# Kernel tuning notes

Hardware: AMD Instinct MI355X
Metric: run time of the kernel (lower is better)

The kernel has to match this reference:

```python
import jax, jax.numpy as jnp
import numpy as np

WH, WW = 14, 14
NUM_HEADS = 12
HEAD_DIM = 64
HIDDEN = NUM_HEADS * HEAD_DIM
SEQ = WH * WW + 1  # 197, includes cls token
NUM_REL = (2 * WH - 1) * (2 * WW - 1) + 3  # 732


def _relative_position_index(wh, ww):
    # Static numpy computation, identical to BeitRelativePositionBias buffer
    coords = np.stack(np.meshgrid(np.arange(wh), np.arange(ww), indexing='ij'))  # [2, wh, ww]
    flat = coords.reshape(2, -1)  # [2, wh*ww]
    rel = flat[:, :, None] - flat[:, None, :]  # [2, N, N]
    rel = rel.transpose(1, 2, 0).astype(np.int64)  # [N, N, 2]
    rel[..., 0] += wh - 1
    rel[..., 1] += ww - 1
    rel[..., 0] *= 2 * ww - 1
    nrd = (2 * wh - 1) * (2 * ww - 1) + 3
    idx = np.zeros((wh * ww + 1, wh * ww + 1), dtype=np.int64)
    idx[1:, 1:] = rel.sum(-1)
    idx[0, :] = nrd - 3
    idx[:, 0] = nrd - 2
    idx[0, 0] = nrd - 1
    return idx

_REL_IDX = jnp.asarray(_relative_position_index(WH, WW))  # [SEQ, SEQ]


def setup_inputs() -> dict:
    key = jax.random.key(0)
    ks = jax.random.split(key, 7)
    B = 64
    s = 1.0 / np.sqrt(HIDDEN)
    return {
        'hidden_states': jax.random.normal(ks[0], (B, SEQ, HIDDEN), jnp.float32),
        'Wq': jax.random.normal(ks[1], (HIDDEN, HIDDEN), jnp.float32) * s,
        'bq': jax.random.normal(ks[2], (HIDDEN,), jnp.float32) * 0.02,
        'Wk': jax.random.normal(ks[3], (HIDDEN, HIDDEN), jnp.float32) * s,
        'Wv': jax.random.normal(ks[4], (HIDDEN, HIDDEN), jnp.float32) * s,
        'bv': jax.random.normal(ks[5], (HIDDEN,), jnp.float32) * 0.02,
        'bias_table': jax.random.normal(ks[6], (NUM_REL, NUM_HEADS), jnp.float32) * 0.02,
    }


def reference(hidden_states, Wq, bq, Wk, Wv, bv, bias_table):
    B, S, D = hidden_states.shape
    H, Dh = NUM_HEADS, HEAD_DIM

    def heads(x):  # [B,S,D] -> [B,H,S,Dh]
        return x.reshape(B, S, H, Dh).transpose(0, 2, 1, 3)

    q = heads(hidden_states @ Wq + bq)
    k = heads(hidden_states @ Wk)           # key projection has no bias
    v = heads(hidden_states @ Wv + bv)

    scores = jnp.einsum('bhqd,bhkd->bhqk', q, k) / jnp.sqrt(jnp.float32(Dh))
    # relative position bias: gather [SEQ,SEQ,H] -> [H,SEQ,SEQ]
    rel_bias = bias_table[_REL_IDX].transpose(2, 0, 1)
    scores = scores + rel_bias[None]

    probs = jax.nn.softmax(scores, axis=-1)  # dropout prob = 0 (eval)
    ctx = jnp.einsum('bhqk,bhkd->bhqd', probs, v)
    ctx = ctx.transpose(0, 2, 1, 3).reshape(B, S, D)
    return ctx
```

## Files before the change

### kernel.cpp

```cpp
#include <hip/hip_runtime.h>
#include <hip/hip_bf16.h>
#include <stdint.h>

typedef unsigned short u16;
typedef __attribute__((ext_vector_type(4))) float f32x4;
typedef __attribute__((ext_vector_type(8))) short s16x8;
typedef __attribute__((ext_vector_type(4))) unsigned short u16x4;
typedef __attribute__((ext_vector_type(4))) float fvec4;

#define NH 12
#define DH 64
#define HID 768
#define SEQ 197
#define VP 224
#define NREL 732
#define BATCH 64
#define MROWS (BATCH*SEQ)
#define NCAT (3*HID)
#define BK 64
#define MT 99
#define NT 18
#define NWG (MT*NT)
#define AWG (768*13)
#define QKSTRIDE (SEQ*DH)

#define PB_X 4728
#define PB_W (PB_X + 432)
#define PB_B (PB_W + 9)
#define PB_E (PB_B + 2028)

static __device__ __forceinline__ u16 f2bf(float f) {
  union { float f; uint32_t u; } v; v.f = f;
  uint32_t u = v.u;
  return (u16)((u + 0x7FFFu + ((u >> 16) & 1u)) >> 16);
}
static __device__ __forceinline__ float bf2f(u16 v) {
  union { uint32_t u; float f; } x; x.u = ((uint32_t)v) << 16; return x.f;
}

__global__ __launch_bounds__(256) void prep_all(const float* __restrict__ x,
                                                const float* __restrict__ Wq, const float* __restrict__ Wk,
                                                const float* __restrict__ Wv, const float* __restrict__ bq,
                                                const float* __restrict__ bv, const float* __restrict__ btab,
                                                u16* __restrict__ xb, u16* __restrict__ Wt,
                                                float* __restrict__ bc, u16* __restrict__ Bxt) {
  __shared__ float t[64][65];
  const int bi = blockIdx.x;
  const int tid = threadIdx.x;
  if (bi < PB_X) {
    int i = bi * 256 + tid;
    fvec4 a = ((const fvec4*)x)[2 * i];
    fvec4 b = ((const fvec4*)x)[2 * i + 1];
    s16x8 r;
    r[0] = (short)f2bf(a[0]); r[1] = (short)f2bf(a[1]); r[2] = (short)f2bf(a[2]); r[3] = (short)f2bf(a[3]);
    r[4] = (short)f2bf(b[0]); r[5] = (short)f2bf(b[1]); r[6] = (short)f2bf(b[2]); r[7] = (short)f2bf(b[3]);
    ((s16x8*)xb)[i] = r;
  } else if (bi < PB_W) {
    int f = bi - PB_X;
    int n0 = (f % 36) * 64, k0 = (f / 36) * 64;
    int m = n0 / HID;
    const float* W = (m == 0) ? Wq : ((m == 1) ? Wk : Wv);
    int nn0 = n0 - m * HID;
    for (int i = tid; i < 64 * 64; i += 256) {
      int r = i >> 6, c = i & 63;
      t[r][c] = W[(size_t)(k0 + r) * HID + nn0 + c];
    }
    __syncthreads();
    for (int i = tid; i < 64 * 64; i += 256) {
      int r = i >> 6, c = i & 63;
      Wt[(size_t)(n0 + r) * HID + k0 + c] = f2bf(t[c][r]);
    }
  } else if (bi < PB_B) {
    int i = (bi - PB_W) * 256 + tid;
    if (i < NCAT) {
      int m = i / HID, r = i - m * HID;
      bc[i] = (m == 0) ? bq[r] : ((m == 2) ? bv[r] : 0.f);
    }
  } else {
    int i = (bi - PB_B) * 256 + tid;
    int h = i / (208 * 208);
    int r = i - h * 208 * 208;
    int k = r / 208, q = r - k * 208;
    float v;
    if (k >= SEQ) v = -1e30f;
    else if (q >= SEQ) v = 0.f;
    else {
      int idx;
      if (q == 0) idx = (k == 0) ? 731 : 729;
      else if (k == 0) idx = 730;
      else {
        int iq = (q - 1) / 14, jq = (q - 1) % 14;
        int ik = (k - 1) / 14, jk = (k - 1) % 14;
        idx = (iq - ik + 13) * 27 + (jq - jk + 13);
      }
      v = btab[(size_t)idx * NH + h];
    }
    Bxt[i] = f2bf(v);
  }
}

static __device__ __forceinline__ void stage128(const u16* __restrict__ gbase, int grow0, int growmax,
                                                u16* lds, int w, int l) {
#pragma unroll
  for (int i = 0; i < 4; ++i) {
    int ch = w * 4 + i;
    int r = ch * 8 + (l >> 3);
    int grow = grow0 + r; if (grow > growmax) grow = growmax;
    int c = (l & 7) ^ (l >> 3);
    const u16* g = gbase + (size_t)grow * HID + c * 8;
    __builtin_amdgcn_global_load_lds((const __attribute__((address_space(1))) void*)g,
                                     (__attribute__((address_space(3))) void*)(lds + ch * 512),
                                     16, 0, 0);
  }
}

static __device__ __forceinline__ void compute128(const u16* As, const u16* Bs, int wr, int wc,
                                                  int li, int lg, f32x4 acc[4][4]) {
#pragma unroll
  for (int kk = 0; kk < 2; ++kk) {
    s16x8 af[4], bf[4];
#pragma unroll
    for (int mi = 0; mi < 4; ++mi) {
      int r = wr * 64 + mi * 16 + li;
      int c = (kk * 4 + lg) ^ (r & 7);
      af[mi] = *(const s16x8*)((const char*)As + r * 128 + c * 16);
    }
#pragma unroll
    for (int ni = 0; ni < 4; ++ni) {
      int r = wc * 64 + ni * 16 + li;
      int c = (kk * 4 + lg) ^ (r & 7);
      bf[ni] = *(const s16x8*)((const char*)Bs + r * 128 + c * 16);
    }
#pragma unroll
    for (int mi = 0; mi < 4; ++mi)
#pragma unroll
      for (int ni = 0; ni < 4; ++ni)
        acc[mi][ni] = __builtin_amdgcn_mfma_f32_16x16x32_bf16(af[mi], bf[ni], acc[mi][ni], 0, 0, 0);
  }
}

__global__ __launch_bounds__(256, 2) void qkv_gemm(const u16* __restrict__ Xb, const u16* __restrict__ Wt,
                                                   const float* __restrict__ bc, u16* __restrict__ Qw,
                                                   u16* __restrict__ Kw, u16* __restrict__ Vt) {
  __shared__ u16 LDSU[32768];
  u16* As0 = LDSU;
  u16* Bs0 = LDSU + 8192;
  u16* As1 = LDSU + 16384;
  u16* Bs1 = LDSU + 24576;
  const int tid = threadIdx.x;
  const int w = tid >> 6, l = tid & 63;
  const int wr = w >> 1, wc = w & 1;
  const int lg = l >> 4, li = l & 15;

  const int lin = blockIdx.x;
  const int xcd = lin & 7;
  const int pos = lin >> 3;
  const int work = (xcd < 6 ? xcd * 223 : 6 * 223 + (xcd - 6) * 222) + pos;
  const int mt = work / NT, nt = work - mt * NT;
  const int arow0 = mt * 128, brow0 = nt * 128;

  f32x4 acc[4][4] = {};

  stage128(Xb, arow0, MROWS - 1, As0, w, l);
  stage128(Wt, brow0, NCAT - 1, Bs0, w, l);
  __syncthreads();

  for (int kt2 = 0; kt2 < 6; ++kt2) {
    const int kt = kt2 * 2;
    stage128(Xb + (kt + 1) * BK, arow0, MROWS - 1, As1, w, l);
    stage128(Wt + (kt + 1) * BK, brow0, NCAT - 1, Bs1, w, l);
    compute128(As0, Bs0, wr, wc, li, lg, acc);
    __syncthreads();
    if (kt2 < 5) {
      stage128(Xb + (kt + 2) * BK, arow0, MROWS - 1, As0, w, l);
      stage128(Wt + (kt + 2) * BK, brow0, NCAT - 1, Bs0, w, l);
    }
    compute128(As1, Bs1, wr, wc, li, lg, acc);
    __syncthreads();
  }

  const int mblk = nt / 6;
  float bcv[4];
#pragma unroll
  for (int ni = 0; ni < 4; ++ni) bcv[ni] = bc[brow0 + wc * 64 + ni * 16 + li];

  if (mblk < 2) {
    u16* __restrict__ dst = (mblk == 0) ? Qw : Kw;
    const float scale = (mblk == 0) ? 0.125f : 1.0f;
    int hv[4], dv[4];
#pragma unroll
    for (int ni = 0; ni < 4; ++ni) {
      int cloc = brow0 - mblk * HID + wc * 64 + ni * 16 + li;
      hv[ni] = cloc >> 6; dv[ni] = cloc & 63;
    }
#pragma unroll
    for (int mi = 0; mi < 4; ++mi) {
#pragma unroll
      for (int j = 0; j < 4; ++j) {
        int row = arow0 + wr * 64 + mi * 16 + lg * 4 + j;
        if (row < MROWS) {
          int b = row / SEQ, s = row - b * SEQ;
#pragma unroll
          for (int ni = 0; ni < 4; ++ni)
            dst[((size_t)(b * NH + hv[ni]) * SEQ + s) * DH + dv[ni]] = f2bf((acc[mi][ni][j] + bcv[ni]) * scale);
        }
      }
    }
  } else {
#pragma unroll
    for (int mi = 0; mi < 4; ++mi) {
#pragma unroll
      for (int ni = 0; ni < 4; ++ni) {
        u16x4 pk;
#pragma unroll
        for (int j = 0; j < 4; ++j) pk[j] = f2bf(acc[mi][ni][j] + bcv[ni]);
        *(u16x4*)&LDSU[w * 4352 + (ni * 16 + li) * 68 + mi * 16 + lg * 4] = pk;
      }
    }
    __syncthreads();
    const int cw0 = brow0 - 2 * HID;
#pragma unroll 4
    for (int p = 0; p < 64; ++p) {
      int i = p * 256 + tid;
      int r = i & 127, c = i >> 7;
      int wq = ((r >> 6) << 1) | (c >> 6);
      u16 v = LDSU[wq * 4352 + (c & 63) * 68 + (r & 63)];
      int row = arow0 + r;
      if (row < MROWS) {
        int b = row / SEQ, s = row - b * SEQ;
        int cl = cw0 + c;
        int h = cl >> 6, d = cl & 63;
        Vt[((size_t)(b * NH + h) * DH + d) * VP + s] = v;
      }
    }
  }
}

__global__ __launch_bounds__(64, 3) void attn(const u16* __restrict__ Qw, const u16* __restrict__ Kw,
                                              const u16* __restrict__ Vt, const u16* __restrict__ Bxt,
                                              float* __restrict__ out) {
  __shared__ u16 P[16 * 232];
  const int l = threadIdx.x;
  const int lg = l >> 4, li = l & 15;
  const int lin = blockIdx.x;
  const int work = (lin & 7) * (AWG / 8) + (lin >> 3);
  const int bh = work / 13, qf = work - bh * 13;
  const int b = bh / NH, h = bh - b * NH;

  for (int t = l; t < 16 * 24; t += 64) {
    int rr = t / 24, cc = t - rr * 24;
    P[rr * 232 + 208 + cc] = 0;
  }

  const u16* Qb = Qw + (size_t)bh * QKSTRIDE;
  const u16* Kb = Kw + (size_t)bh * QKSTRIDE;
  const u16* Vb = Vt + (size_t)bh * DH * VP;
  const u16* Bhp = Bxt + (size_t)h * 208 * 208 + qf * 16 + lg * 4;

  s16x8 a0 = *(const s16x8*)(Qb + (size_t)(qf * 16 + li) * DH + lg * 8);
  s16x8 a1 = *(const s16x8*)(Qb + (size_t)(qf * 16 + li) * DH + 32 + lg * 8);

  u16x4 bb[13];
#pragma unroll
  for (int kf = 0; kf < 13; ++kf)
    bb[kf] = *(const u16x4*)(Bhp + (size_t)(kf * 16 + li) * 208);

  s16x8 kb0[3], kb1[3];
#pragma unroll
  for (int p = 0; p < 3; ++p) {
    kb0[p] = *(const s16x8*)(Kb + (size_t)(p * 16 + li) * DH + lg * 8);
    kb1[p] = *(const s16x8*)(Kb + (size_t)(p * 16 + li) * DH + 32 + lg * 8);
  }
  f32x4 S[13];
#pragma unroll
  for (int kf = 0; kf < 13; ++kf) {
    const int slot = kf % 3;
    f32x4 c = {};
    c = __builtin_amdgcn_mfma_f32_16x16x32_bf16(a0, kb0[slot], c, 0, 0, 0);
    c = __builtin_amdgcn_mfma_f32_16x16x32_bf16(a1, kb1[slot], c, 0, 0, 0);
    if (kf + 3 < 13) {
      kb0[slot] = *(const s16x8*)(Kb + (size_t)((kf + 3) * 16 + li) * DH + lg * 8);
      kb1[slot] = *(const s16x8*)(Kb + (size_t)((kf + 3) * 16 + li) * DH + 32 + lg * 8);
    }
#pragma unroll
    for (int j = 0; j < 4; ++j)
      S[kf][j] = c[j] + bf2f(bb[kf][j]);
  }

  float rinv[4];
#pragma unroll
  for (int j = 0; j < 4; ++j) {
    float m = S[0][j];
#pragma unroll
    for (int kf = 1; kf < 13; ++kf) m = fmaxf(m, S[kf][j]);
    m = fmaxf(m, __shfl_xor(m, 1));
    m = fmaxf(m, __shfl_xor(m, 2));
    m = fmaxf(m, __shfl_xor(m, 4));
    m = fmaxf(m, __shfl_xor(m, 8));
    float sum = 0.f;
#pragma unroll
    for (int kf = 0; kf < 13; ++kf) {
      float p = __expf(S[kf][j] - m);
      S[kf][j] = p;
      sum += p;
    }
    sum += __shfl_xor(sum, 1);
    sum += __shfl_xor(sum, 2);
    sum += __shfl_xor(sum, 4);
    sum += __shfl_xor(sum, 8);
    rinv[j] = 1.0f / sum;
  }

#pragma unroll
  for (int kf = 0; kf < 13; ++kf)
#pragma unroll
    for (int j = 0; j < 4; ++j)
      P[(lg * 4 + j) * 232 + kf * 16 + li] = f2bf(S[kf][j]);

  s16x8 vb[4];
#pragma unroll
  for (int p = 0; p < 4; ++p)
    vb[p] = *(const s16x8*)(Vb + (size_t)((p / 7) * 16 + li) * VP + (p % 7) * 32 + lg * 8);
  f32x4 o[4];
#pragma unroll
  for (int nf = 0; nf < 4; ++nf) {
    f32x4 c = {};
#pragma unroll
    for (int t = 0; t < 7; ++t) {
      const int u = nf * 7 + t, slot = u & 3;
      s16x8 pa = *(const s16x8*)(&P[li * 232 + t * 32 + lg * 8]);
      c = __builtin_amdgcn_mfma_f32_16x16x32_bf16(pa, vb[slot], c, 0, 0, 0);
      if (u + 4 < 28) {
        const int u2 = u + 4;
        vb[slot] = *(const s16x8*)(Vb + (size_t)((u2 / 7) * 16 + li) * VP + (u2 % 7) * 32 + lg * 8);
      }
    }
    o[nf] = c;
  }
#pragma unroll
  for (int nf = 0; nf < 4; ++nf) {
#pragma unroll
    for (int j = 0; j < 4; ++j) {
      int q = qf * 16 + lg * 4 + j;
      if (q < SEQ)
        out[((size_t)(b * SEQ + q)) * HID + h * DH + nf * 16 + li] = o[nf][j] * rinv[j];
    }
  }
}

extern "C" void kernel_launch(void* const* d_in, const int* in_sizes, int n_in,
                              void* d_out, int out_size, void* d_ws, size_t ws_size,
                              hipStream_t stream) {
  const float* hidden = (const float*)d_in[0];
  const float* Wq = (const float*)d_in[1];
  const float* bq = (const float*)d_in[2];
  const float* Wk = (const float*)d_in[3];
  const float* Wv = (const float*)d_in[4];
  const float* bv = (const float*)d_in[5];
  const float* btab = (const float*)d_in[6];
  float* out = (float*)d_out;

  char* ws = (char*)d_ws;
  u16* Xb  = (u16*)(ws);
  u16* Wt  = (u16*)(ws + 19365888);
  float* bc = (float*)(ws + 22904832);
  u16* Bxt = (u16*)(ws + 22914048);
  u16* Qw  = (u16*)(ws + 23952512);
  u16* Kw  = (u16*)(ws + 43322496);
  u16* Vt  = (u16*)(ws + 62692480);

  prep_all<<<dim3(PB_E), dim3(256), 0, stream>>>(hidden, Wq, Wk, Wv, bq, bv, btab, Xb, Wt, bc, Bxt);
  qkv_gemm<<<dim3(NWG), dim3(256), 0, stream>>>(Xb, Wt, bc, Qw, Kw, Vt);
  attn<<<dim3(AWG), dim3(64), 0, stream>>>(Qw, Kw, Vt, Bxt, out);
}
```

Measured before the change: 135.7 us.

## Share K across query tiles via swizzled LDS in per-head attention blocks

The attention kernel now launches one 2-wave block per (batch, head) instead of one single-wave block per (batch, head, query tile). The whole K matrix for the head is staged once into LDS with direct global-to-LDS loads and an XOR swizzle. Each wave then loops over its query tiles, reading K from LDS rather than re-fetching it from global memory for every tile. This removes redundant K traffic, but it cuts the grid to 768 small blocks and serialises query tiles within each wave, which lowers occupancy and latency hiding.

```diff
diff --git a/kernel.cpp b/kernel.cpp
--- a/kernel.cpp
+++ b/kernel.cpp
@@ -21,7 +21,6 @@
 #define MT 99
 #define NT 18
 #define NWG (MT*NT)
-#define AWG (768*13)
 #define QKSTRIDE (SEQ*DH)
 
 #define PB_X 4728
@@ -236,114 +235,124 @@
   }
 }
 
-__global__ __launch_bounds__(64, 3) void attn(const u16* __restrict__ Qw, const u16* __restrict__ Kw,
-                                              const u16* __restrict__ Vt, const u16* __restrict__ Bxt,
-                                              float* __restrict__ out) {
-  __shared__ u16 P[16 * 232];
-  const int l = threadIdx.x;
+__global__ __launch_bounds__(128, 2) void attn(const u16* __restrict__ Qw, const u16* __restrict__ Kw,
+                                               const u16* __restrict__ Vt, const u16* __restrict__ Bxt,
+                                               float* __restrict__ out) {
+  __shared__ u16 Klds[208 * 64];
+  __shared__ u16 P[2][16 * 232];
+  const int tid = threadIdx.x;
+  const int w = tid >> 6, l = tid & 63;
   const int lg = l >> 4, li = l & 15;
   const int lin = blockIdx.x;
-  const int work = (lin & 7) * (AWG / 8) + (lin >> 3);
-  const int bh = work / 13, qf = work - bh * 13;
+  const int bh = (lin & 7) * 96 + (lin >> 3);
   const int b = bh / NH, h = bh - b * NH;
-
-  for (int t = l; t < 16 * 24; t += 64) {
-    int rr = t / 24, cc = t - rr * 24;
-    P[rr * 232 + 208 + cc] = 0;
-  }
 
   const u16* Qb = Qw + (size_t)bh * QKSTRIDE;
   const u16* Kb = Kw + (size_t)bh * QKSTRIDE;
   const u16* Vb = Vt + (size_t)bh * DH * VP;
-  const u16* Bhp = Bxt + (size_t)h * 208 * 208 + qf * 16 + lg * 4;
-
-  s16x8 a0 = *(const s16x8*)(Qb + (size_t)(qf * 16 + li) * DH + lg * 8);
-  s16x8 a1 = *(const s16x8*)(Qb + (size_t)(qf * 16 + li) * DH + 32 + lg * 8);
-
-  u16x4 bb[13];
-#pragma unroll
-  for (int kf = 0; kf < 13; ++kf)
-    bb[kf] = *(const u16x4*)(Bhp + (size_t)(kf * 16 + li) * 208);
-
-  s16x8 kb0[3], kb1[3];
-#pragma unroll
-  for (int p = 0; p < 3; ++p) {
-    kb0[p] = *(const s16x8*)(Kb + (size_t)(p * 16 + li) * DH + lg * 8);
-    kb1[p] = *(const s16x8*)(Kb + (size_t)(p * 16 + li) * DH + 32 + lg * 8);
-  }
-  f32x4 S[13];
-#pragma unroll
-  for (int kf = 0; kf < 13; ++kf) {
-    const int slot = kf % 3;
-    f32x4 c = {};
-    c = __builtin_amdgcn_mfma_f32_16x16x32_bf16(a0, kb0[slot], c, 0, 0, 0);
-    c = __builtin_amdgcn_mfma_f32_16x16x32_bf16(a1, kb1[slot], c, 0, 0, 0);
-    if (kf + 3 < 13) {
-      kb0[slot] = *(const s16x8*)(Kb + (size_t)((kf + 3) * 16 + li) * DH + lg * 8);
-      kb1[slot] = *(const s16x8*)(Kb + (size_t)((kf + 3) * 16 + li) * DH + 32 + lg * 8);
-    }
-#pragma unroll
-    for (int j = 0; j < 4; ++j)
-      S[kf][j] = c[j] + bf2f(bb[kf][j]);
-  }
-
-  float rinv[4];
-#pragma unroll
-  for (int j = 0; j < 4; ++j) {
-    float m = S[0][j];
-#pragma unroll
-    for (int kf = 1; kf < 13; ++kf) m = fmaxf(m, S[kf][j]);
-    m = fmaxf(m, __shfl_xor(m, 1));
-    m = fmaxf(m, __shfl_xor(m, 2));
-    m = fmaxf(m, __shfl_xor(m, 4));
-    m = fmaxf(m, __shfl_xor(m, 8));
-    float sum = 0.f;
+
+#pragma unroll
+  for (int i = 0; i < 13; ++i) {
+    int ch = (w * 13 + i) * 64 + l;
+    int r = ch >> 3, c = ch & 7;
+    int sc = c ^ (r & 7);
+    __builtin_amdgcn_global_load_lds((const __attribute__((address_space(1))) void*)
+                                         (Kb + (size_t)r * DH + sc * 8),
+                                     (__attribute__((address_space(3))) void*)(Klds + (size_t)ch * 8),
+                                     16, 0, 0);
+  }
+  for (int t = l; t < 16 * 24; t += 64) {
+    int rr = t / 24, cc = t - rr * 24;
+    P[w][rr * 232 + 208 + cc] = 0;
+  }
+  __syncthreads();
+
+  for (int it = 0; it < 7; ++it) {
+    const int qf = w + 2 * it;
+    if (qf >= 13) break;
+
+    const u16* Bhp = Bxt + (size_t)h * 208 * 208 + qf * 16 + lg * 4;
+
+    s16x8 a0 = *(const s16x8*)(Qb + (size_t)(qf * 16 + li) * DH + lg * 8);
+    s16x8 a1 = *(const s16x8*)(Qb + (size_t)(qf * 16 + li) * DH + 32 + lg * 8);
+
+    u16x4 bb[13];
+#pragma unroll
+    for (int kf = 0; kf < 13; ++kf)
+      bb[kf] = *(const u16x4*)(Bhp + (size_t)(kf * 16 + li) * 208);
+
+    f32x4 S[13];
 #pragma unroll
     for (int kf = 0; kf < 13; ++kf) {
-      float p = __expf(S[kf][j] - m);
-      S[kf][j] = p;
-      sum += p;
-    }
-    sum += __shfl_xor(sum, 1);
-    sum += __shfl_xor(sum, 2);
-    sum += __shfl_xor(sum, 4);
-    sum += __shfl_xor(sum, 8);
-    rinv[j] = 1.0f / sum;
-  }
-
-#pragma unroll
-  for (int kf = 0; kf < 13; ++kf)
-#pragma unroll
-    for (int j = 0; j < 4; ++j)
-      P[(lg * 4 + j) * 232 + kf * 16 + li] = f2bf(S[kf][j]);
-
-  s16x8 vb[4];
-#pragma unroll
-  for (int p = 0; p < 4; ++p)
-    vb[p] = *(const s16x8*)(Vb + (size_t)((p / 7) * 16 + li) * VP + (p % 7) * 32 + lg * 8);
-  f32x4 o[4];
-#pragma unroll
-  for (int nf = 0; nf < 4; ++nf) {
-    f32x4 c = {};
-#pragma unroll
-    for (int t = 0; t < 7; ++t) {
-      const int u = nf * 7 + t, slot = u & 3;
-      s16x8 pa = *(const s16x8*)(&P[li * 232 + t * 32 + lg * 8]);
-      c = __builtin_amdgcn_mfma_f32_16x16x32_bf16(pa, vb[slot], c, 0, 0, 0);
-      if (u + 4 < 28) {
-        const int u2 = u + 4;
-        vb[slot] = *(const s16x8*)(Vb + (size_t)((u2 / 7) * 16 + li) * VP + (u2 % 7) * 32 + lg * 8);
-      }
-    }
-    o[nf] = c;
-  }
-#pragma unroll
-  for (int nf = 0; nf < 4; ++nf) {
+      int r = kf * 16 + li;
+      s16x8 k0 = *(const s16x8*)((const char*)Klds + r * 128 + ((lg) ^ (r & 7)) * 16);
+      s16x8 k1 = *(const s16x8*)((const char*)Klds + r * 128 + ((4 + lg) ^ (r & 7)) * 16);
+      f32x4 c = {};
+      c = __builtin_amdgcn_mfma_f32_16x16x32_bf16(a0, k0, c, 0, 0, 0);
+      c = __builtin_amdgcn_mfma_f32_16x16x32_bf16(a1, k1, c, 0, 0, 0);
+#pragma unroll
+      for (int j = 0; j < 4; ++j)
+        S[kf][j] = c[j] + bf2f(bb[kf][j]);
+    }
+
+    float rinv[4];
 #pragma unroll
     for (int j = 0; j < 4; ++j) {
-      int q = qf * 16 + lg * 4 + j;
-      if (q < SEQ)
-        out[((size_t)(b * SEQ + q)) * HID + h * DH + nf * 16 + li] = o[nf][j] * rinv[j];
+      float m = S[0][j];
+#pragma unroll
+      for (int kf = 1; kf < 13; ++kf) m = fmaxf(m, S[kf][j]);
+      m = fmaxf(m, __shfl_xor(m, 1));
+      m = fmaxf(m, __shfl_xor(m, 2));
+      m = fmaxf(m, __shfl_xor(m, 4));
+      m = fmaxf(m, __shfl_xor(m, 8));
+      float sum = 0.f;
+#pragma unroll
+      for (int kf = 0; kf < 13; ++kf) {
+        float p = __expf(S[kf][j] - m);
+        S[kf][j] = p;
+        sum += p;
+      }
+      sum += __shfl_xor(sum, 1);
+      sum += __shfl_xor(sum, 2);
+      sum += __shfl_xor(sum, 4);
+      sum += __shfl_xor(sum, 8);
+      rinv[j] = 1.0f / sum;
+    }
+
+#pragma unroll
+    for (int kf = 0; kf < 13; ++kf)
+#pragma unroll
+      for (int j = 0; j < 4; ++j)
+        P[w][(lg * 4 + j) * 232 + kf * 16 + li] = f2bf(S[kf][j]);
+
+    s16x8 vb[4];
+#pragma unroll
+    for (int p = 0; p < 4; ++p)
+      vb[p] = *(const s16x8*)(Vb + (size_t)((p / 7) * 16 + li) * VP + (p % 7) * 32 + lg * 8);
+    f32x4 o[4];
+#pragma unroll
+    for (int nf = 0; nf < 4; ++nf) {
+      f32x4 c = {};
+#pragma unroll
+      for (int t = 0; t < 7; ++t) {
+        const int u = nf * 7 + t, slot = u & 3;
+        s16x8 pa = *(const s16x8*)(&P[w][li * 232 + t * 32 + lg * 8]);
+        c = __builtin_amdgcn_mfma_f32_16x16x32_bf16(pa, vb[slot], c, 0, 0, 0);
+        if (u + 4 < 28) {
+          const int u2 = u + 4;
+          vb[slot] = *(const s16x8*)(Vb + (size_t)((u2 / 7) * 16 + li) * VP + (u2 % 7) * 32 + lg * 8);
+        }
+      }
+      o[nf] = c;
+    }
+#pragma unroll
+    for (int nf = 0; nf < 4; ++nf) {
+#pragma unroll
+      for (int j = 0; j < 4; ++j) {
+        int q = qf * 16 + lg * 4 + j;
+        if (q < SEQ)
+          out[((size_t)(b * SEQ + q)) * HID + h * DH + nf * 16 + li] = o[nf][j] * rinv[j];
+      }
     }
   }
 }
@@ -371,5 +380,5 @@
 
   prep_all<<<dim3(PB_E), dim3(256), 0, stream>>>(hidden, Wq, Wk, Wv, bq, bv, btab, Xb, Wt, bc, Bxt);
   qkv_gemm<<<dim3(NWG), dim3(256), 0, stream>>>(Xb, Wt, bc, Qw, Kw, Vt);
-  attn<<<dim3(AWG), dim3(64), 0, stream>>>(Qw, Kw, Vt, Bxt, out);
-}
+  attn<<<dim3(768), dim3(128), 0, stream>>>(Qw, Kw, Vt, Bxt, out);
+}
```

Result: faster. 119.0 us (-12.3%).
